# Kernel tuning notes

Hardware: AMD Instinct MI355X
Metric: run time of the kernel (lower is better)

## Reference

```python
import jax, jax.numpy as jnp
import numpy as np

N, E, C, B = 8192, 131072, 128, 64


def sph_l012(v):
    # real spherical harmonics l=0,1,2, component normalization, input NOT normalized
    x, y, z = v[:, 0], v[:, 1], v[:, 2]
    r2 = x * x + y * y + z * z
    s3, s15, s5 = 3.0 ** 0.5, 15.0 ** 0.5, 5.0 ** 0.5
    l0 = jnp.ones_like(x)[:, None]
    l1 = s3 * v
    l2 = jnp.stack([s15 * x * y, s15 * y * z, 0.5 * s5 * (3.0 * z * z - r2),
                    s15 * x * z, 0.5 * s15 * (x * x - y * y)], axis=-1)
    return jnp.concatenate([l0, l1, l2], axis=-1)  # (E, 9)


def sph_norm(sh, w):
    # per-degree RMS norm with learnable per-degree scale (layer_norm_sh style)
    eps = 1e-6
    outs = []
    for li, (lo, hi) in enumerate([(0, 1), (1, 4), (4, 9)]):
        blk = sh[:, lo:hi]
        rms = jnp.sqrt(jnp.mean(blk * blk, axis=-1, keepdims=True) + eps)
        outs.append(blk / rms * w[li])
    return jnp.concatenate(outs, axis=-1)


def layernorm(x, w, b):
    mu = jnp.mean(x, axis=-1, keepdims=True)
    var = jnp.mean((x - mu) ** 2, axis=-1, keepdims=True)
    return (x - mu) / jnp.sqrt(var + 1e-5) * w + b


def seg_mean(vals, idx, num):
    s = jax.ops.segment_sum(vals, idx, num_segments=num)
    cnt = jax.ops.segment_sum(jnp.ones((vals.shape[0],), vals.dtype), idx, num_segments=num)
    cnt = jnp.maximum(cnt, 1.0).reshape((num,) + (1,) * (vals.ndim - 1))
    return s / cnt


def setup_inputs() -> dict:
    key = jax.random.key(0)
    ks = jax.random.split(key, 10)
    sc = 1.0 / np.sqrt(C)
    return {
        "node_emb": jax.random.normal(ks[0], (N, 9, C), jnp.float32),
        "edge_distance_vec": jax.random.normal(ks[1], (E, 3), jnp.float32),
        "edge_index": jax.random.randint(ks[2], (2, E), 0, N),
        "batch": jnp.sort(jax.random.randint(ks[3], (N,), 0, B)),
        "sph_w": jnp.ones((3,), jnp.float32),
        "ln_w": jnp.ones((C,), jnp.float32),
        "ln_b": jnp.zeros((C,), jnp.float32),
        "W1": jax.random.normal(ks[4], (C, C), jnp.float32) * sc,
        "b1": jnp.zeros((C,), jnp.float32),
        "W2": jax.random.normal(ks[5], (C, 1), jnp.float32) * sc,
        "b2": jnp.zeros((1,), jnp.float32),
    }


def reference(node_emb, edge_distance_vec, edge_index, batch, sph_w, ln_w, ln_b, W1, b1, W2, b2):
    # spherical-harmonic edge weights (detached in original)
    sh = jax.lax.stop_gradient(sph_l012(edge_distance_vec))          # (E, 9)
    sh = sph_norm(sh, sph_w)                                         # (E, 9)
    # gather target-node embeddings and contract over sh components
    x_edge = node_emb[edge_index[1]]                                 # (E, 9, C)
    x_edge = jnp.einsum('elc,el->ec', x_edge, sh)                    # (E, C)
    x_edge = layernorm(x_edge, ln_w, ln_b)
    # rank-2 outer product per edge
    v = edge_distance_vec
    op = (v[:, :, None] * v[:, None, :]).reshape(E, 9)               # (E, 9)
    edge_outer = x_edge[:, :, None] * op[:, None, :]                 # (E, C, 9)
    # scatter-mean to nodes, then node-level MLP (edge_level=False)
    node_outer = seg_mean(edge_outer, edge_index[1], N)              # (N, C, 9)
    node_outer = jnp.swapaxes(node_outer, 1, 2)                      # (N, 9, C)
    h = jax.nn.silu(node_outer @ W1 + b1)                            # (N, 9, C)
    node_out = (h @ W2 + b2).reshape(N, 9)                           # (N, 9)
    # intensive pooling over graphs (extensive=False)
    r2 = seg_mean(node_out, batch, B)                                # (B, 9)
    return r2
```

## Files before the change

kernel.cpp:

```cpp
#include <hip/hip_runtime.h>


#define SQ3  1.73205080756887729f
#define SQ15 3.87298334620741688f
#define SQ5  2.23606797749978970f

#define PIDX(l, l2) ((l) * 9 - (l) * ((l) - 1) / 2 + ((l2) - (l)))

__global__ void preproc_kernel(const int* __restrict__ idx1, const int* __restrict__ batch,
                               int* __restrict__ cnt, int* __restrict__ bcnt,
                               int* __restrict__ elist, int slot, int E, int N) {
    int i = blockIdx.x * blockDim.x + threadIdx.x;
    if (i < E) {
        int nn = idx1[i];
        int p = atomicAdd(&cnt[nn], 1);
        if (p < slot) elist[(size_t)nn * slot + p] = i;
    }
    if (i < N) atomicAdd(&bcnt[batch[i]], 1);
}

__device__ const unsigned char d_PL[45] = {
    0,0,0,0,0,0,0,0,0, 1,1,1,1,1,1,1,1, 2,2,2,2,2,2,2, 3,3,3,3,3,3,
    4,4,4,4,4, 5,5,5,5, 6,6,6, 7,7, 8};
__device__ const unsigned char d_PL2[45] = {
    0,1,2,3,4,5,6,7,8, 1,2,3,4,5,6,7,8, 2,3,4,5,6,7,8, 3,4,5,6,7,8,
    4,5,6,7,8, 5,6,7,8, 6,7,8, 7,8, 8};

__global__ __launch_bounds__(256)
void node_kernel(const float* __restrict__ emb, const float* __restrict__ vec,
                 const int* __restrict__ cnt, const int* __restrict__ elist, int slot,
                 const float* __restrict__ sph_w, const float* __restrict__ ln_w,
                 const float* __restrict__ ln_b,
                 const float* __restrict__ W1, const float* __restrict__ b1,
                 const float* __restrict__ W2, const float* __restrict__ b2,
                 const int* __restrict__ batch, float* __restrict__ r2s)
{
    const int n = blockIdx.x;
    const int t = threadIdx.x;

    __shared__ float emb_s[9][133];
    __shared__ float stats_p[54][2];
    __shared__ float stats[54];
    __shared__ float sred[64][68];
    __shared__ float stats2[66];
    __shared__ float no_s[128][8];
    __shared__ float mlp2[128][6];
    __shared__ float red2[2][6];

    const int   cntn = cnt[n];
    const int   cnE  = min(cntn, slot);
    const float invc = 1.f / (float)(cntn > 0 ? cntn : 1);
    const float inv128 = 1.f / 128.f;

    const float* eb = emb + (size_t)n * 1152;
    for (int i4 = t; i4 < 288; i4 += 256) {
        const float4 v4 = *(const float4*)(eb + i4 * 4);
        const int flat = i4 * 4, row = flat >> 7, col = flat & 127;
        emb_s[row][col + 0] = v4.x; emb_s[row][col + 1] = v4.y;
        emb_s[row][col + 2] = v4.z; emb_s[row][col + 3] = v4.w;
    }
    __syncthreads();

    {
        const int h = t >> 7, item = t & 127;
        if (item < 54) {
            const int cbeg = h * 64;
            float s = 0.f;
            if (item < 9) {
                for (int c = 0; c < 64; ++c) s += emb_s[item][cbeg + c];
            } else {
                const int l = d_PL[item - 9], l2 = d_PL2[item - 9];
                for (int c = 0; c < 64; ++c)
                    s += emb_s[l][cbeg + c] * emb_s[l2][cbeg + c];
            }
            stats_p[item][h] = s;
        }
    }
    __syncthreads();
    if (t < 54) stats[t] = stats_p[t][0] + stats_p[t][1];
    __syncthreads();

    if (t < cnE) {
        const int e = elist[(size_t)n * slot + t];
        const float vx = vec[e * 3 + 0];
        const float vy = vec[e * 3 + 1];
        const float vz = vec[e * 3 + 2];
        const float rr = vx * vx + vy * vy + vz * vz;

        const float a1x = SQ3 * vx, a1y = SQ3 * vy, a1z = SQ3 * vz;
        const float q0 = SQ15 * vx * vy;
        const float q1 = SQ15 * vy * vz;
        const float q2 = 0.5f * SQ5 * (3.f * vz * vz - rr);
        const float q3 = SQ15 * vx * vz;
        const float q4 = 0.5f * SQ15 * (vx * vx - vy * vy);
        const float inv1 = sph_w[1] * rsqrtf((a1x*a1x + a1y*a1y + a1z*a1z) * (1.f/3.f) + 1e-6f);
        const float inv2 = sph_w[2] * rsqrtf((q0*q0 + q1*q1 + q2*q2 + q3*q3 + q4*q4) * (1.f/5.f) + 1e-6f);

        float sh[9];
        sh[0] = sph_w[0] * rsqrtf(1.0f + 1e-6f);
        sh[1] = a1x * inv1; sh[2] = a1y * inv1; sh[3] = a1z * inv1;
        sh[4] = q0 * inv2;  sh[5] = q1 * inv2;  sh[6] = q2 * inv2;
        sh[7] = q3 * inv2;  sh[8] = q4 * inv2;

        float mu = 0.f;
        #pragma unroll
        for (int l = 0; l < 9; ++l) mu += sh[l] * stats[l];
        mu *= inv128;

        float x2 = 0.f;
        #pragma unroll
        for (int l = 0; l < 9; ++l) {
            x2 += stats[9 + PIDX(l, l)] * sh[l] * sh[l];
            #pragma unroll
            for (int l2 = l + 1; l2 < 9; ++l2)
                x2 += 2.f * stats[9 + PIDX(l, l2)] * sh[l] * sh[l2];
        }
        x2 *= inv128;

        const float var  = x2 - mu * mu;
        const float rinv = rsqrtf(var + 1e-5f);

        float t1[9];
        #pragma unroll
        for (int l = 0; l < 9; ++l) t1[l] = rinv * sh[l];

        const float op[6] = {vx*vx, vx*vy, vx*vz, vy*vy, vy*vz, vz*vz};
        const float mru = rinv * mu;
        #pragma unroll
        for (int u = 0; u < 6; ++u) {
            const float o = op[u];
            #pragma unroll
            for (int l = 0; l < 9; ++l) sred[t][u * 9 + l] = o * t1[l];
            sred[t][54 + u] = o * mru;
            sred[t][60 + u] = o;
        }
    }
    __syncthreads();

    if (t < 66) {
        float s = 0.f;
        for (int e = 0; e < cnE; ++e) s += sred[e][t];
        stats2[t] = s;
    }
    __syncthreads();

    {
        const int c = t & 127, ug = (t >> 7) * 3;
        const float lwc = ln_w[c], lbc = ln_b[c];
        #pragma unroll
        for (int du = 0; du < 3; ++du) {
            const int u = ug + du;
            float a = 0.f;
            #pragma unroll
            for (int l = 0; l < 9; ++l) a += emb_s[l][c] * stats2[u * 9 + l];
            no_s[c][u] = (lwc * (a - stats2[54 + u]) + lbc * stats2[60 + u]) * invc;
        }
    }
    __syncthreads();

    const int k = t & 127, h2 = t >> 7;
    float hh[6];
    #pragma unroll
    for (int u = 0; u < 6; ++u) hh[u] = 0.f;
    {
        const float* w1p = W1 + (size_t)(h2 * 64) * 128 + k;
        const int cbase = h2 * 64;
        #pragma unroll 4
        for (int cc = 0; cc < 64; ++cc) {
            const float w = w1p[cc * 128];
            const float4 nv  = *(const float4*)&no_s[cbase + cc][0];
            const float2 nv2 = *(const float2*)&no_s[cbase + cc][4];
            hh[0] += nv.x  * w; hh[1] += nv.y  * w; hh[2] += nv.z * w;
            hh[3] += nv.w  * w; hh[4] += nv2.x * w; hh[5] += nv2.y * w;
        }
    }
    if (h2) {
        #pragma unroll
        for (int u = 0; u < 6; ++u) mlp2[k][u] = hh[u];
    }
    __syncthreads();
    if (t < 128) {
        const float b1k = b1[k], w2k = W2[k];
        float sv[6];
        #pragma unroll
        for (int u = 0; u < 6; ++u) {
            const float hv = hh[u] + mlp2[k][u] + b1k;
            const float sg = 1.f / (1.f + expf(-hv));
            sv[u] = hv * sg * w2k;
        }
        #pragma unroll
        for (int u = 0; u < 6; ++u) {
            #pragma unroll
            for (int o = 32; o >= 1; o >>= 1) sv[u] += __shfl_xor(sv[u], o);
        }
        if ((t & 63) == 0) {
            #pragma unroll
            for (int u = 0; u < 6; ++u) red2[t >> 6][u] = sv[u];
        }
    }
    __syncthreads();
    if (t < 9) {
        const int umap[9] = {0, 1, 2, 1, 3, 4, 2, 4, 5};
        const float tot = red2[0][umap[t]] + red2[1][umap[t]] + b2[0];
        atomicAdd(&r2s[batch[n] * 9 + t], tot);
    }
}

__global__ void finalize_kernel(const float* __restrict__ r2s, const int* __restrict__ bcnt,
                                float* __restrict__ out, int M) {
    int i = blockIdx.x * blockDim.x + threadIdx.x;
    if (i < M) {
        int b = i / 9;
        int cb = bcnt[b];
        out[i] = r2s[i] / (float)(cb > 0 ? cb : 1);
    }
}

extern "C" void kernel_launch(void* const* d_in, const int* in_sizes, int n_in,
                              void* d_out, int out_size, void* d_ws, size_t ws_size,
                              hipStream_t stream) {
    const float* emb   = (const float*)d_in[0];
    const float* vec   = (const float*)d_in[1];
    const int*   eidx  = (const int*)  d_in[2];
    const int*   batch = (const int*)  d_in[3];
    const float* sph_w = (const float*)d_in[4];
    const float* ln_w  = (const float*)d_in[5];
    const float* ln_b  = (const float*)d_in[6];
    const float* W1    = (const float*)d_in[7];
    const float* b1    = (const float*)d_in[8];
    const float* W2    = (const float*)d_in[9];
    const float* b2    = (const float*)d_in[10];

    const int N = in_sizes[3];
    const int E = in_sizes[1] / 3;
    const int B = out_size / 9;
    const int* idx1 = eidx + E;

    int*   cnt   = (int*)d_ws;
    int*   bcnt  = cnt + N;
    float* r2s   = (float*)(bcnt + B);
    int*   elist = (int*)(r2s + B * 9);

    const size_t fixed = (size_t)(N + B + B * 9) * 4;
    int slot = 64;
    if (ws_size < fixed + (size_t)N * slot * 4) {
        size_t avail = (ws_size > fixed) ? (ws_size - fixed) / ((size_t)N * 4) : 1;
        slot = (int)avail;
        if (slot > 64) slot = 64;
        if (slot < 1)  slot = 1;
    }

    hipMemsetAsync(cnt, 0, fixed, stream);

    const int threads = 256;
    const int gp = (max(E, N) + threads - 1) / threads;
    preproc_kernel<<<gp, threads, 0, stream>>>(idx1, batch, cnt, bcnt, elist, slot, E, N);
    node_kernel<<<N, 256, 0, stream>>>(emb, vec, cnt, elist, slot,
                                       sph_w, ln_w, ln_b, W1, b1, W2, b2,
                                       batch, r2s);
    finalize_kernel<<<(B * 9 + 255) / 256, 256, 0, stream>>>(r2s, bcnt, (float*)d_out, B * 9);
}
```

Measured before the change: 144.0 us.

## Process one node per wavefront with DPP reductions and block barriers removed

Restructures node_kernel so each 64-lane wavefront handles a whole node, with four nodes per block. The embedding rows stay in registers, statistics are reduced with DPP cross-lane sums, and wave-level fences replace block-wide __syncthreads. The W1 matvec becomes per-lane float2 columns with six accumulators each, and the edge-stat reduction becomes a product of compact per-edge rows. The preprocessing kernel also loads edge indices as int4, four per thread. This trades more registers per lane and some serial per-wave work for fewer barriers and less shared-memory traffic.

Result: slower. 185.7 us (+29.0%).

```diff
diff --git a/kernel.cpp b/kernel.cpp
--- a/kernel.cpp
+++ b/kernel.cpp
@@ -5,26 +5,43 @@
 #define SQ15 3.87298334620741688f
 #define SQ5  2.23606797749978970f
 
-#define PIDX(l, l2) ((l) * 9 - (l) * ((l) - 1) / 2 + ((l2) - (l)))
+__device__ __forceinline__ float dpp_sum64(float v) {
+    int x;
+    x = __builtin_amdgcn_update_dpp(0, __float_as_int(v), 0x111, 0xF, 0xF, true); v += __int_as_float(x);
+    x = __builtin_amdgcn_update_dpp(0, __float_as_int(v), 0x112, 0xF, 0xF, true); v += __int_as_float(x);
+    x = __builtin_amdgcn_update_dpp(0, __float_as_int(v), 0x114, 0xF, 0xF, true); v += __int_as_float(x);
+    x = __builtin_amdgcn_update_dpp(0, __float_as_int(v), 0x118, 0xF, 0xF, true); v += __int_as_float(x);
+    x = __builtin_amdgcn_update_dpp(0, __float_as_int(v), 0x142, 0xA, 0xF, true); v += __int_as_float(x);
+    x = __builtin_amdgcn_update_dpp(0, __float_as_int(v), 0x143, 0xC, 0xF, true); v += __int_as_float(x);
+    return v;
+}
+
+__device__ __forceinline__ void wave_fence() {
+    __builtin_amdgcn_wave_barrier();
+    asm volatile("" ::: "memory");
+}
 
 __global__ void preproc_kernel(const int* __restrict__ idx1, const int* __restrict__ batch,
                                int* __restrict__ cnt, int* __restrict__ bcnt,
                                int* __restrict__ elist, int slot, int E, int N) {
-    int i = blockIdx.x * blockDim.x + threadIdx.x;
-    if (i < E) {
-        int nn = idx1[i];
-        int p = atomicAdd(&cnt[nn], 1);
-        if (p < slot) elist[(size_t)nn * slot + p] = i;
+    const int i = blockIdx.x * blockDim.x + threadIdx.x;
+    const int i4 = i * 4;
+    if (i4 + 3 < E) {
+        const int4 v = *(const int4*)&idx1[i4];
+        int p;
+        p = atomicAdd(&cnt[v.x], 1); if (p < slot) elist[(size_t)v.x * slot + p] = i4;
+        p = atomicAdd(&cnt[v.y], 1); if (p < slot) elist[(size_t)v.y * slot + p] = i4 + 1;
+        p = atomicAdd(&cnt[v.z], 1); if (p < slot) elist[(size_t)v.z * slot + p] = i4 + 2;
+        p = atomicAdd(&cnt[v.w], 1); if (p < slot) elist[(size_t)v.w * slot + p] = i4 + 3;
+    } else {
+        for (int k = i4; k < E; ++k) {
+            const int nn = idx1[k];
+            const int p = atomicAdd(&cnt[nn], 1);
+            if (p < slot) elist[(size_t)nn * slot + p] = k;
+        }
     }
     if (i < N) atomicAdd(&bcnt[batch[i]], 1);
 }
-
-__device__ const unsigned char d_PL[45] = {
-    0,0,0,0,0,0,0,0,0, 1,1,1,1,1,1,1,1, 2,2,2,2,2,2,2, 3,3,3,3,3,3,
-    4,4,4,4,4, 5,5,5,5, 6,6,6, 7,7, 8};
-__device__ const unsigned char d_PL2[45] = {
-    0,1,2,3,4,5,6,7,8, 1,2,3,4,5,6,7,8, 2,3,4,5,6,7,8, 3,4,5,6,7,8,
-    4,5,6,7,8, 5,6,7,8, 6,7,8, 7,8, 8};
 
 __global__ __launch_bounds__(256)
 void node_kernel(const float* __restrict__ emb, const float* __restrict__ vec,
@@ -33,55 +50,52 @@
                  const float* __restrict__ ln_b,
                  const float* __restrict__ W1, const float* __restrict__ b1,
                  const float* __restrict__ W2, const float* __restrict__ b2,
-                 const int* __restrict__ batch, float* __restrict__ r2s)
+                 const int* __restrict__ batch, float* __restrict__ r2s, int N)
 {
-    const int n = blockIdx.x;
-    const int t = threadIdx.x;
-
-    __shared__ float emb_s[9][133];
-    __shared__ float stats_p[54][2];
-    __shared__ float stats[54];
-    __shared__ float sred[64][68];
-    __shared__ float stats2[66];
-    __shared__ float no_s[128][8];
-    __shared__ float mlp2[128][6];
-    __shared__ float red2[2][6];
+    const int lane = threadIdx.x & 63;
+    const int wv   = threadIdx.x >> 6;
+    const int n    = blockIdx.x * 4 + wv;
+    if (n >= N) return;
+
+    __shared__ float escr[4][64][20];
+    __shared__ float statsL[4][56];
+    __shared__ float stats2[4][68];
+    __shared__ float noT[4][6][128];
 
     const int   cntn = cnt[n];
     const int   cnE  = min(cntn, slot);
     const float invc = 1.f / (float)(cntn > 0 ? cntn : 1);
     const float inv128 = 1.f / 128.f;
 
+    const int c0 = lane, c1 = lane + 64;
     const float* eb = emb + (size_t)n * 1152;
-    for (int i4 = t; i4 < 288; i4 += 256) {
-        const float4 v4 = *(const float4*)(eb + i4 * 4);
-        const int flat = i4 * 4, row = flat >> 7, col = flat & 127;
-        emb_s[row][col + 0] = v4.x; emb_s[row][col + 1] = v4.y;
-        emb_s[row][col + 2] = v4.z; emb_s[row][col + 3] = v4.w;
-    }
-    __syncthreads();
-
-    {
-        const int h = t >> 7, item = t & 127;
-        if (item < 54) {
-            const int cbeg = h * 64;
-            float s = 0.f;
-            if (item < 9) {
-                for (int c = 0; c < 64; ++c) s += emb_s[item][cbeg + c];
-            } else {
-                const int l = d_PL[item - 9], l2 = d_PL2[item - 9];
-                for (int c = 0; c < 64; ++c)
-                    s += emb_s[l][cbeg + c] * emb_s[l2][cbeg + c];
+    float er0[9], er1[9];
+    #pragma unroll
+    for (int l = 0; l < 9; ++l) { er0[l] = eb[l * 128 + c0]; er1[l] = eb[l * 128 + c1]; }
+
+    const float spw0 = sph_w[0], spw1 = sph_w[1], spw2 = sph_w[2];
+
+    {
+        #pragma unroll
+        for (int l = 0; l < 9; ++l) {
+            const float tot = dpp_sum64(er0[l] + er1[l]);
+            if (lane == 63) statsL[wv][l] = tot;
+        }
+        int idx = 9;
+        #pragma unroll
+        for (int l = 0; l < 9; ++l) {
+            #pragma unroll
+            for (int l2 = l; l2 < 9; ++l2) {
+                const float tot = dpp_sum64(er0[l] * er0[l2] + er1[l] * er1[l2]);
+                if (lane == 63) statsL[wv][idx] = tot;
+                ++idx;
             }
-            stats_p[item][h] = s;
-        }
-    }
-    __syncthreads();
-    if (t < 54) stats[t] = stats_p[t][0] + stats_p[t][1];
-    __syncthreads();
-
-    if (t < cnE) {
-        const int e = elist[(size_t)n * slot + t];
+        }
+    }
+    wave_fence();
+
+    if (lane < cnE) {
+        const int e = elist[(size_t)n * slot + lane];
         const float vx = vec[e * 3 + 0];
         const float vy = vec[e * 3 + 1];
         const float vz = vec[e * 3 + 2];
@@ -93,116 +107,139 @@
         const float q2 = 0.5f * SQ5 * (3.f * vz * vz - rr);
         const float q3 = SQ15 * vx * vz;
         const float q4 = 0.5f * SQ15 * (vx * vx - vy * vy);
-        const float inv1 = sph_w[1] * rsqrtf((a1x*a1x + a1y*a1y + a1z*a1z) * (1.f/3.f) + 1e-6f);
-        const float inv2 = sph_w[2] * rsqrtf((q0*q0 + q1*q1 + q2*q2 + q3*q3 + q4*q4) * (1.f/5.f) + 1e-6f);
+        const float inv1 = spw1 * rsqrtf((a1x*a1x + a1y*a1y + a1z*a1z) * (1.f/3.f) + 1e-6f);
+        const float inv2 = spw2 * rsqrtf((q0*q0 + q1*q1 + q2*q2 + q3*q3 + q4*q4) * (1.f/5.f) + 1e-6f);
 
         float sh[9];
-        sh[0] = sph_w[0] * rsqrtf(1.0f + 1e-6f);
+        sh[0] = spw0 * rsqrtf(1.0f + 1e-6f);
         sh[1] = a1x * inv1; sh[2] = a1y * inv1; sh[3] = a1z * inv1;
         sh[4] = q0 * inv2;  sh[5] = q1 * inv2;  sh[6] = q2 * inv2;
         sh[7] = q3 * inv2;  sh[8] = q4 * inv2;
 
         float mu = 0.f;
         #pragma unroll
-        for (int l = 0; l < 9; ++l) mu += sh[l] * stats[l];
+        for (int l = 0; l < 9; ++l) mu += sh[l] * statsL[wv][l];
         mu *= inv128;
 
         float x2 = 0.f;
-        #pragma unroll
-        for (int l = 0; l < 9; ++l) {
-            x2 += stats[9 + PIDX(l, l)] * sh[l] * sh[l];
-            #pragma unroll
-            for (int l2 = l + 1; l2 < 9; ++l2)
-                x2 += 2.f * stats[9 + PIDX(l, l2)] * sh[l] * sh[l2];
+        {
+            int idx = 9;
+            #pragma unroll
+            for (int l = 0; l < 9; ++l) {
+                #pragma unroll
+                for (int l2 = l; l2 < 9; ++l2) {
+                    const float coef = (l == l2) ? 1.f : 2.f;
+                    x2 += statsL[wv][idx] * (coef * sh[l] * sh[l2]);
+                    ++idx;
+                }
+            }
         }
         x2 *= inv128;
 
         const float var  = x2 - mu * mu;
         const float rinv = rsqrtf(var + 1e-5f);
 
-        float t1[9];
-        #pragma unroll
-        for (int l = 0; l < 9; ++l) t1[l] = rinv * sh[l];
-
-        const float op[6] = {vx*vx, vx*vy, vx*vz, vy*vy, vy*vz, vz*vz};
-        const float mru = rinv * mu;
+        const float4 wA = {rinv*sh[0], rinv*sh[1], rinv*sh[2], rinv*sh[3]};
+        const float4 wB = {rinv*sh[4], rinv*sh[5], rinv*sh[6], rinv*sh[7]};
+        const float4 wC = {rinv*sh[8], rinv*mu, vx*vx, vx*vy};
+        const float4 wD = {vx*vz, vy*vy, vy*vz, vz*vz};
+        *(float4*)&escr[wv][lane][0]  = wA;
+        *(float4*)&escr[wv][lane][4]  = wB;
+        *(float4*)&escr[wv][lane][8]  = wC;
+        *(float4*)&escr[wv][lane][12] = wD;
+        escr[wv][lane][16] = 1.0f;
+    }
+    wave_fence();
+
+    {
+        int a, b;
+        const int j = lane;
+        if (j < 54)      { a = j % 9;          b = 10 + j / 9; }
+        else if (j < 60) { a = 9;              b = 10 + (j - 54); }
+        else             { a = 10 + (j - 60);  b = 16; }
+        const int a2 = 14 + (lane & 1);
+
+        float s = 0.f, s2 = 0.f;
+        for (int e = 0; e < cnE; ++e) {
+            const float* row = &escr[wv][e][0];
+            s  += row[a] * row[b];
+            s2 += row[a2];
+        }
+        stats2[wv][lane] = s;
+        if (lane < 2) stats2[wv][64 + lane] = s2;
+    }
+    wave_fence();
+
+    {
+        const float lw0 = ln_w[c0], lb0 = ln_b[c0];
+        const float lw1 = ln_w[c1], lb1 = ln_b[c1];
         #pragma unroll
         for (int u = 0; u < 6; ++u) {
-            const float o = op[u];
-            #pragma unroll
-            for (int l = 0; l < 9; ++l) sred[t][u * 9 + l] = o * t1[l];
-            sred[t][54 + u] = o * mru;
-            sred[t][60 + u] = o;
-        }
-    }
-    __syncthreads();
-
-    if (t < 66) {
-        float s = 0.f;
-        for (int e = 0; e < cnE; ++e) s += sred[e][t];
-        stats2[t] = s;
-    }
-    __syncthreads();
-
-    {
-        const int c = t & 127, ug = (t >> 7) * 3;
-        const float lwc = ln_w[c], lbc = ln_b[c];
-        #pragma unroll
-        for (int du = 0; du < 3; ++du) {
-            const int u = ug + du;
-            float a = 0.f;
-            #pragma unroll
-            for (int l = 0; l < 9; ++l) a += emb_s[l][c] * stats2[u * 9 + l];
-            no_s[c][u] = (lwc * (a - stats2[54 + u]) + lbc * stats2[60 + u]) * invc;
-        }
-    }
-    __syncthreads();
-
-    const int k = t & 127, h2 = t >> 7;
-    float hh[6];
+            float a0 = 0.f, a1 = 0.f;
+            #pragma unroll
+            for (int l = 0; l < 9; ++l) {
+                const float s1v = stats2[wv][9 * u + l];
+                a0 += er0[l] * s1v;
+                a1 += er1[l] * s1v;
+            }
+            const float S2u = stats2[wv][54 + u];
+            const float S3u = stats2[wv][60 + u];
+            noT[wv][u][c0] = (lw0 * (a0 - S2u) + lb0 * S3u) * invc;
+            noT[wv][u][c1] = (lw1 * (a1 - S2u) + lb1 * S3u) * invc;
+        }
+    }
+    wave_fence();
+
+    float2 hh[6];
     #pragma unroll
-    for (int u = 0; u < 6; ++u) hh[u] = 0.f;
-    {
-        const float* w1p = W1 + (size_t)(h2 * 64) * 128 + k;
-        const int cbase = h2 * 64;
-        #pragma unroll 4
-        for (int cc = 0; cc < 64; ++cc) {
-            const float w = w1p[cc * 128];
-            const float4 nv  = *(const float4*)&no_s[cbase + cc][0];
-            const float2 nv2 = *(const float2*)&no_s[cbase + cc][4];
-            hh[0] += nv.x  * w; hh[1] += nv.y  * w; hh[2] += nv.z * w;
-            hh[3] += nv.w  * w; hh[4] += nv2.x * w; hh[5] += nv2.y * w;
-        }
-    }
-    if (h2) {
-        #pragma unroll
-        for (int u = 0; u < 6; ++u) mlp2[k][u] = hh[u];
-    }
-    __syncthreads();
-    if (t < 128) {
-        const float b1k = b1[k], w2k = W2[k];
+    for (int u = 0; u < 6; ++u) { hh[u].x = 0.f; hh[u].y = 0.f; }
+    {
+        const float* w1base = W1 + 2 * lane;
+        for (int c4 = 0; c4 < 32; ++c4) {
+            float4 nv[6];
+            #pragma unroll
+            for (int u = 0; u < 6; ++u) nv[u] = *(const float4*)&noT[wv][u][c4 * 4];
+            #pragma unroll
+            for (int cc = 0; cc < 4; ++cc) {
+                const float2 w = *(const float2*)(w1base + (size_t)(c4 * 4 + cc) * 128);
+                #pragma unroll
+                for (int u = 0; u < 6; ++u) {
+                    const float s = ((const float*)&nv[u])[cc];
+                    hh[u].x = fmaf(s, w.x, hh[u].x);
+                    hh[u].y = fmaf(s, w.y, hh[u].y);
+                }
+            }
+        }
+    }
+
+    {
+        const float2 b1v = *(const float2*)&b1[2 * lane];
+        const float2 w2v = *(const float2*)&W2[2 * lane];
         float sv[6];
         #pragma unroll
         for (int u = 0; u < 6; ++u) {
-            const float hv = hh[u] + mlp2[k][u] + b1k;
-            const float sg = 1.f / (1.f + expf(-hv));
-            sv[u] = hv * sg * w2k;
-        }
-        #pragma unroll
-        for (int u = 0; u < 6; ++u) {
-            #pragma unroll
-            for (int o = 32; o >= 1; o >>= 1) sv[u] += __shfl_xor(sv[u], o);
-        }
-        if ((t & 63) == 0) {
-            #pragma unroll
-            for (int u = 0; u < 6; ++u) red2[t >> 6][u] = sv[u];
-        }
-    }
-    __syncthreads();
-    if (t < 9) {
-        const int umap[9] = {0, 1, 2, 1, 3, 4, 2, 4, 5};
-        const float tot = red2[0][umap[t]] + red2[1][umap[t]] + b2[0];
-        atomicAdd(&r2s[batch[n] * 9 + t], tot);
+            const float zx = hh[u].x + b1v.x;
+            const float zy = hh[u].y + b1v.y;
+            const float gx = zx / (1.f + __expf(-zx));
+            const float gy = zy / (1.f + __expf(-zy));
+            sv[u] = gx * w2v.x + gy * w2v.y;
+        }
+        float tot[6];
+        #pragma unroll
+        for (int u = 0; u < 6; ++u) tot[u] = dpp_sum64(sv[u]);
+        if (lane == 63) {
+            const float bb = b2[0];
+            const int base = batch[n] * 9;
+            atomicAdd(&r2s[base + 0], tot[0] + bb);
+            atomicAdd(&r2s[base + 1], tot[1] + bb);
+            atomicAdd(&r2s[base + 2], tot[2] + bb);
+            atomicAdd(&r2s[base + 3], tot[1] + bb);
+            atomicAdd(&r2s[base + 4], tot[3] + bb);
+            atomicAdd(&r2s[base + 5], tot[4] + bb);
+            atomicAdd(&r2s[base + 6], tot[2] + bb);
+            atomicAdd(&r2s[base + 7], tot[4] + bb);
+            atomicAdd(&r2s[base + 8], tot[5] + bb);
+        }
     }
 }
 
@@ -252,11 +289,12 @@
 
     hipMemsetAsync(cnt, 0, fixed, stream);
 
-    const int threads = 256;
-    const int gp = (max(E, N) + threads - 1) / threads;
-    preproc_kernel<<<gp, threads, 0, stream>>>(idx1, batch, cnt, bcnt, elist, slot, E, N);
-    node_kernel<<<N, 256, 0, stream>>>(emb, vec, cnt, elist, slot,
-                                       sph_w, ln_w, ln_b, W1, b1, W2, b2,
-                                       batch, r2s);
+    const int pthreads = 256;
+    const int pwork = max((E + 3) / 4, N);
+    preproc_kernel<<<(pwork + pthreads - 1) / pthreads, pthreads, 0, stream>>>(
+        idx1, batch, cnt, bcnt, elist, slot, E, N);
+    node_kernel<<<(N + 3) / 4, 256, 0, stream>>>(emb, vec, cnt, elist, slot,
+                                                 sph_w, ln_w, ln_b, W1, b1, W2, b2,
+                                                 batch, r2s, N);
     finalize_kernel<<<(B * 9 + 255) / 256, 256, 0, stream>>>(r2s, bcnt, (float*)d_out, B * 9);
 }
```
